# Optimization experiments

Measured on AMD Instinct MI355X. Metric: run time of the kernel, lower is better.

The kernel has to match this reference:

```python
import jax, jax.numpy as jnp
import numpy as np

STRIDE = 1
KSIZE = 3
DEMOD = True


def _conv_single(xi, wi, pad):
    # xi: [C,H,W], wi: [O,C,k,k] -> [O,H,W]
    out = jax.lax.conv_general_dilated(
        xi[None], wi, window_strides=(STRIDE, STRIDE),
        padding=[(pad, pad), (pad, pad)],
        dimension_numbers=("NCHW", "OIHW", "NCHW"))
    return out[0]


def setup_inputs() -> dict:
    key = jax.random.key(0)
    ks = jax.random.split(key, 6)
    B, Cin, Cout, S, H, W = 8, 512, 512, 512, 64, 64
    return {
        "x": jax.random.normal(ks[0], (B, Cin, H, W), jnp.float32),
        "y": jax.random.normal(ks[1], (B, S), jnp.float32),
        "affine_w": jax.random.normal(ks[2], (Cin, S), jnp.float32) * 0.02,
        "affine_b": jax.random.normal(ks[3], (Cin,), jnp.float32) * 0.02,
        "weight": jax.random.normal(ks[4], (Cout, Cin, KSIZE, KSIZE), jnp.float32) * 0.05,
        "bias": jax.random.normal(ks[5], (1, Cout, 1, 1), jnp.float32) * 0.02,
    }


def reference(x, y, affine_w, affine_b, weight, bias):
    B, _, H, W = x.shape
    style_dim = affine_w.shape[1]
    coef = 1.0 / np.sqrt(style_dim)  # ELR: gain / sqrt(fan_in)
    # style modulation scale per input channel: [B, Cin]
    s = (y * coef) @ affine_w.T + affine_b + 1.0
    # per-sample weights: [B, O, I, k, k]
    w = weight[None, :, :, :, :] * s[:, None, :, None, None]
    if DEMOD:
        d = jax.lax.rsqrt(jnp.sum(w * w, axis=(2, 3, 4), keepdims=True) + 1e-4)
        w = w * d
    pad = ((H - 1) * (STRIDE - 1) + (KSIZE - 1)) // 2
    out = jax.vmap(lambda xi, wi: _conv_single(xi, wi, pad))(x, w)  # [B,O,H,W]
    return out + bias
```

## Files before the change

kernel.cpp:

```cpp
#include <hip/hip_runtime.h>

typedef __attribute__((ext_vector_type(8))) short short8;
typedef __attribute__((ext_vector_type(4))) float floatx4;
typedef unsigned short u16;
typedef unsigned int u32;

#define NB 8
#define CI 512
#define CO 512
#define HH 64
#define WW 64
#define HP 66
#define WP 66
#define BK 64

__device__ __forceinline__ u16 f2bf(float f) {
  u32 u = __builtin_bit_cast(u32, f);
  u += 0x7fffu + ((u >> 16) & 1u);
  return (u16)(u >> 16);
}

__device__ __forceinline__ void gload16(const void* g, void* l) {
  __builtin_amdgcn_global_load_lds(
      (const __attribute__((address_space(1))) unsigned int*)g,
      (__attribute__((address_space(3))) unsigned int*)l, 16, 0, 0);
}

__global__ __launch_bounds__(256) void k_prep1(
    const float* __restrict__ y, const float* __restrict__ aw,
    const float* __restrict__ ab, float* __restrict__ s,
    const float* __restrict__ wt, float* __restrict__ wsum,
    u16* __restrict__ wbv)
{
  if (blockIdx.x < 1024) {
    const int wid = blockIdx.x * 4 + (threadIdx.x >> 6);
    const int lane = threadIdx.x & 63;
    const int b = wid >> 9, i = wid & 511;
    float sum = 0.f;
    #pragma unroll
    for (int j = 0; j < 8; ++j) {
      const int k = lane + (j << 6);
      sum += y[b * CI + k] * aw[i * CI + k];
    }
    #pragma unroll
    for (int off = 32; off; off >>= 1) sum += __shfl_xor(sum, off);
    if (lane == 0) s[wid] = sum * 0.044194173824159216f + ab[i] + 1.0f;
  } else {
    const int idx = (blockIdx.x - 1024) * 256 + threadIdx.x;
    const int i = idx & 511;
    const int o = idx >> 9;
    const float* p = wt + (size_t)idx * 9;
    float v[9];
    float sum = 0.f;
    #pragma unroll
    for (int t = 0; t < 9; ++t) { v[t] = p[t]; sum += v[t] * v[t]; }
    wsum[idx] = sum;
    #pragma unroll
    for (int t = 0; t < 9; ++t) wbv[(((o * 9 + t) << 9) | i)] = f2bf(v[t]);
  }
}

__global__ __launch_bounds__(256) void k_xfd(
    const float* __restrict__ x, const float* __restrict__ s,
    u16* __restrict__ xs, const float* __restrict__ wsum,
    float* __restrict__ d)
{
  __shared__ __align__(16) u16 lds[64 * 72];
  if (blockIdx.x >= 4096) {
    const int wid = (blockIdx.x - 4096) * 4 + (threadIdx.x >> 6);
    const int lane = threadIdx.x & 63;
    const int b = wid >> 9, o = wid & 511;
    float sum = 0.f;
    #pragma unroll
    for (int j = 0; j < 8; ++j) {
      const int i = lane + (j << 6);
      const float sv = s[b * CI + i];
      sum += wsum[o * CI + i] * sv * sv;
    }
    #pragma unroll
    for (int off = 32; off; off >>= 1) sum += __shfl_xor(sum, off);
    if (lane == 0) d[wid] = rsqrtf(sum + 1e-4f);
    return;
  }
  const int blk = blockIdx.x;
  const int ic = blk & 7;
  const int h = (blk >> 3) & 63;
  const int b = blk >> 9;
  const int i0 = ic << 6;
  const int t = threadIdx.x;
  const int w = t & 63;
  const int i4 = t >> 6;
  #pragma unroll
  for (int p = 0; p < 16; ++p) {
    const int ii = i4 + (p << 2);
    const float xv = x[((size_t)(b * CI + i0 + ii) * HH + h) * WW + w];
    const float sv = s[b * CI + i0 + ii];
    lds[w * 72 + ii] = f2bf(xv * sv);
  }
  const uint4 z4 = {0u, 0u, 0u, 0u};
  if (t < 16) {
    const int wside = (t < 8) ? 0 : 65;
    const int q = t & 7;
    *(uint4*)&xs[((size_t)(b * HP + h + 1) * WP + wside) * CI + i0 + (q << 3)] = z4;
  }
  if (h == 0) {
    for (int idx = t; idx < 2 * 66 * 8; idx += 256) {
      const int row = (idx < 528) ? 0 : 65;
      const int rem = (idx < 528) ? idx : idx - 528;
      const int wz = rem >> 3;
      const int q = rem & 7;
      *(uint4*)&xs[((size_t)(b * HP + row) * WP + wz) * CI + i0 + (q << 3)] = z4;
    }
  }
  __syncthreads();
  const int w2 = t >> 2;
  const int q = t & 3;
  const uint4* src = (const uint4*)&lds[w2 * 72 + (q << 4)];
  const uint4 v0 = src[0];
  const uint4 v1 = src[1];
  u16* dst = xs + ((size_t)(b * HP + h + 1) * WP + (w2 + 1)) * CI + i0 + (q << 4);
  *(uint4*)dst = v0;
  *((uint4*)dst + 1) = v1;
}

__global__ __launch_bounds__(512, 2) void k_conv(
    const u16* __restrict__ xs, const u16* __restrict__ wb,
    const float* __restrict__ dmod, const float* __restrict__ bias,
    float* __restrict__ out)
{
  __shared__ __align__(16) u16 lA[2 * 16384];
  __shared__ __align__(16) u16 lB[2 * 16384];

  const int blk0 = blockIdx.x;
  const int lblk = ((blk0 & 7) << 5) + (blk0 >> 3);
  const int mt = lblk >> 7;
  const int b  = (lblk >> 4) & 7;
  const int nt = lblk & 15;
  const int ob = mt << 8;
  const int p0 = nt << 8;

  const int tid = threadIdx.x;
  const int wid = tid >> 6;
  const int lane = tid & 63;
  const int col = lane & 15;
  const int k8  = lane >> 4;
  const int wr  = wid >> 2;
  const int wc  = wid & 3;

  const int lr = lane >> 3;
  const int ls = lane & 7;
  const int swz = ls ^ lr;

  u32 aoff[4], boff[4], ldst[4];
  #pragma unroll
  for (int h2 = 0; h2 < 4; ++h2) {
    const int rowBase = ((h2 >> 1) << 7) + (wid << 4) + ((h2 & 1) << 3);
    const int rowIdx = rowBase + lr;
    aoff[h2] = (u32)((ob + rowIdx) * 4608 + (swz << 3));
    const int p = p0 + rowIdx;
    boff[h2] = (u32)(((b * HP + (p >> 6)) * WP + (p & 63)) * 512 + (swz << 3));
    ldst[h2] = (u32)(rowBase << 6);
  }

  const u32 sA0 = (u32)(((0 + k8) ^ (col & 7)) << 3);
  const u32 sA1 = (u32)(((4 + k8) ^ (col & 7)) << 3);
  const u32 aRead = (u32)((((wr << 7) + col) << 6));
  const u32 bRead = (u32)((((wc << 6) + col) << 6));

  floatx4 acc[8][4];
  #pragma unroll
  for (int m = 0; m < 8; ++m)
    #pragma unroll
    for (int n = 0; n < 4; ++n)
      acc[m][n] = (floatx4){0.f, 0.f, 0.f, 0.f};

  short8 a0[4][2], b0[2][2], b1[2][2];

#define SA(TILE, H, BUF) do {                                                 \
    const u32 at_ = (u32)((TILE) << 6);                                       \
    gload16(wb + aoff[(H)*2+0] + at_, &lA[((BUF) << 14) + ldst[(H)*2+0]]);    \
    gload16(wb + aoff[(H)*2+1] + at_, &lA[((BUF) << 14) + ldst[(H)*2+1]]);    \
  } while (0)

#define SB(TILE, H, BUF) do {                                                 \
    const int t_ = (TILE);                                                    \
    const int tap_ = t_ >> 3;                                                 \
    const int kh_ = tap_ / 3;                                                 \
    const int kw_ = tap_ - kh_ * 3;                                           \
    const u32 bt_ = (u32)(((kh_ * WP + kw_) << 9) + ((t_ & 7) << 6));         \
    gload16(xs + boff[(H)*2+0] + bt_, &lB[((BUF) << 14) + ldst[(H)*2+0]]);    \
    gload16(xs + boff[(H)*2+1] + bt_, &lB[((BUF) << 14) + ldst[(H)*2+1]]);    \
  } while (0)

#define READ_A(PA, MH) do {                                                   \
    _Pragma("unroll")                                                         \
    for (int mq = 0; mq < 4; ++mq) {                                          \
      a0[mq][0] = *(const short8*)((PA) + (MH) * 4096 + mq * 1024 + sA0);     \
      a0[mq][1] = *(const short8*)((PA) + (MH) * 4096 + mq * 1024 + sA1);     \
    }                                                                         \
  } while (0)

#define READ_B(PB, NH, BV) do {                                               \
    _Pragma("unroll")                                                         \
    for (int nq = 0; nq < 2; ++nq) {                                          \
      BV[nq][0] = *(const short8*)((PB) + (NH) * 2048 + nq * 1024 + sA0);     \
      BV[nq][1] = *(const short8*)((PB) + (NH) * 2048 + nq * 1024 + sA1);     \
    }                                                                         \
  } while (0)

#define MFMA_Q(MH, NH, BV) do {                                               \
    _Pragma("unroll")                                                         \
    for (int kk = 0; kk < 2; ++kk)                                            \
      _Pragma("unroll")                                                       \
      for (int nq = 0; nq < 2; ++nq)                                          \
        _Pragma("unroll")                                                     \
        for (int mq = 0; mq < 4; ++mq)                                        \
          acc[(MH)*4+mq][(NH)*2+nq] = __builtin_amdgcn_mfma_f32_16x16x32_bf16(\
              a0[mq][kk], BV[nq][kk], acc[(MH)*4+mq][(NH)*2+nq], 0, 0, 0);    \
  } while (0)

#define SBAR __builtin_amdgcn_s_barrier()
#define SCH0 __builtin_amdgcn_sched_barrier(0)
#define PRI1 __builtin_amdgcn_s_setprio(1)
#define PRI0 __builtin_amdgcn_s_setprio(0)

#define BODY8(T0, FULL) do {                                                  \
    const u16* pA0 = lA + aRead;                                              \
    const u16* pB0 = lB + bRead;                                              \
    const u16* pA1 = lA + 16384 + aRead;                                      \
    const u16* pB1 = lB + 16384 + bRead;                                      \
                                        \
    READ_A(pA0, 0); READ_B(pB0, 0, b0);                                       \
    SCH0; SA((T0) + 1, 0, 1);                                                 \
    SBAR; PRI1; MFMA_Q(0, 0, b0); PRI0; SBAR;                                 \
                                                          \
    READ_B(pB0, 1, b1);                                                       \
    SCH0; SA((T0) + 1, 1, 1);                                                 \
    SBAR; PRI1; MFMA_Q(0, 1, b1); PRI0; SBAR;                                 \
                           \
    READ_A(pA0, 1);                                                           \
    SCH0; if (FULL) SB((T0) + 2, 0, 0);                                       \
    SBAR; PRI1; MFMA_Q(1, 1, b1); PRI0; SBAR;                                 \
                          \
    SCH0; if (FULL) SB((T0) + 2, 1, 0);                                       \
    SBAR; PRI1; MFMA_Q(1, 0, b0); PRI0;                                       \
    if (FULL) asm volatile("s_waitcnt vmcnt(4)" ::: "memory");                \
    else      asm volatile("s_waitcnt vmcnt(0)" ::: "memory");                \
    SBAR;                                                                     \
       \
    READ_A(pA1, 0); READ_B(pB1, 0, b0);                                       \
    SCH0; if (FULL) SA((T0) + 2, 0, 0);                                       \
    SBAR; PRI1; MFMA_Q(0, 0, b0); PRI0; SBAR;                                 \
                                                          \
    READ_B(pB1, 1, b1);                                                       \
    SCH0; if (FULL) SA((T0) + 2, 1, 0);                                       \
    SBAR; PRI1; MFMA_Q(0, 1, b1); PRI0; SBAR;                                 \
                           \
    READ_A(pA1, 1);                                                           \
    SCH0; if (FULL) SB((T0) + 3, 0, 1);                                       \
    SBAR; PRI1; MFMA_Q(1, 1, b1); PRI0; SBAR;                                 \
                          \
    SCH0; if (FULL) SB((T0) + 3, 1, 1);                                       \
    SBAR; PRI1; MFMA_Q(1, 0, b0); PRI0;                                       \
    if (FULL) asm volatile("s_waitcnt vmcnt(4)" ::: "memory");                \
    SBAR;                                                                     \
  } while (0)

  SB(0, 0, 0); SB(0, 1, 0); SA(0, 0, 0); SA(0, 1, 0);
  SB(1, 0, 1); SB(1, 1, 1);
  asm volatile("s_waitcnt vmcnt(4)" ::: "memory");
  SCH0;
  SBAR;

  for (int j = 0; j < 35; ++j) BODY8(j * 2, 1);
  BODY8(70, 0);

#undef SA
#undef SB
#undef READ_A
#undef READ_B
#undef MFMA_Q
#undef BODY8
#undef SBAR
#undef SCH0
#undef PRI1
#undef PRI0

  #pragma unroll
  for (int m = 0; m < 8; ++m) {
    #pragma unroll
    for (int r = 0; r < 4; ++r) {
      const int o = ob + (wr << 7) + (m << 4) + (k8 << 2) + r;
      const float dm = dmod[b * CO + o];
      const float bs = bias[o];
      float* po = out + (((size_t)(b * CO + o)) << 12) + p0 + (wc << 6);
      #pragma unroll
      for (int n = 0; n < 4; ++n)
        po[(n << 4) + col] = acc[m][n][r] * dm + bs;
    }
  }
}

extern "C" void kernel_launch(void* const* d_in, const int* in_sizes, int n_in,
                              void* d_out, int out_size, void* d_ws, size_t ws_size,
                              hipStream_t stream) {
  const float* x    = (const float*)d_in[0];
  const float* y    = (const float*)d_in[1];
  const float* aw   = (const float*)d_in[2];
  const float* ab   = (const float*)d_in[3];
  const float* wt   = (const float*)d_in[4];
  const float* bias = (const float*)d_in[5];
  float* out = (float*)d_out;

  char* ws = (char*)d_ws;
  const size_t XS_BYTES = (size_t)NB * HP * WP * CI * 2;
  const size_t WB_BYTES = (size_t)CO * 9 * CI * 2;
  const size_t WS_BYTES = (size_t)CO * CI * 4;
  u16* xsb    = (u16*)ws;
  u16* wbuf   = (u16*)(ws + XS_BYTES);
  float* wsum = (float*)(ws + XS_BYTES + WB_BYTES);
  float* sbuf = (float*)(ws + XS_BYTES + WB_BYTES + WS_BYTES);
  float* dbuf = sbuf + NB * CI;

  k_prep1<<<dim3(2048), dim3(256), 0, stream>>>(y, aw, ab, sbuf, wt, wsum, wbuf);
  k_xfd  <<<dim3(5120), dim3(256), 0, stream>>>(x, sbuf, xsb, wsum, dbuf);
  k_conv <<<dim3(256), dim3(512), 0, stream>>>(xsb, wbuf, dbuf, bias, out);
}
```

Measured before the change: 158.9 us.

## Restructure conv main loop into per-tile stages with early B prefetch

Rewrites the unrolled two-tile body into a TILE4 macro parameterised by buffer and mode. The next tile's first B fragment is read from LDS at the end of the current tile, and the vmcnt waits are split into finer stages. The block-index swizzle is also replaced with a plain linear mapping of (nt, mt, b). The aim is to hide LDS read latency before the first MFMA group. In exchange, the finer waits and the different B-buffer ordering risk race or stall issues, and dropping the swizzle may change L2 locality.

```diff
diff --git a/kernel.cpp b/kernel.cpp
--- a/kernel.cpp
+++ b/kernel.cpp
@@ -131,11 +131,10 @@
   __shared__ __align__(16) u16 lA[2 * 16384];
   __shared__ __align__(16) u16 lB[2 * 16384];
 
-  const int blk0 = blockIdx.x;
-  const int lblk = ((blk0 & 7) << 5) + (blk0 >> 3);
-  const int mt = lblk >> 7;
-  const int b  = (lblk >> 4) & 7;
-  const int nt = lblk & 15;
+  const int blk = blockIdx.x;
+  const int nt = blk & 15;
+  const int mt = (blk >> 4) & 1;
+  const int b  = blk >> 5;
   const int ob = mt << 8;
   const int p0 = nt << 8;
 
@@ -224,63 +223,57 @@
 #define PRI1 __builtin_amdgcn_s_setprio(1)
 #define PRI0 __builtin_amdgcn_s_setprio(0)
 
-#define BODY8(T0, FULL) do {                                                  \
-    const u16* pA0 = lA + aRead;                                              \
-    const u16* pB0 = lB + bRead;                                              \
-    const u16* pA1 = lA + 16384 + aRead;                                      \
-    const u16* pB1 = lB + 16384 + bRead;                                      \
-                                        \
-    READ_A(pA0, 0); READ_B(pB0, 0, b0);                                       \
-    SCH0; SA((T0) + 1, 0, 1);                                                 \
+#define TILE4(T, C, MODE) do {                                                \
+    const u16* pA  = lA + ((C) << 14) + aRead;                                \
+    const u16* pB  = lB + ((C) << 14) + bRead;                                \
+    const u16* pBn = lB + ((1 - (C)) << 14) + bRead;                          \
+         \
+    READ_A(pA, 0);                                                            \
+    SCH0; if (MODE >= 1) SA((T) + 1, 0, 1 - (C));                             \
     SBAR; PRI1; MFMA_Q(0, 0, b0); PRI0; SBAR;                                 \
-                                                          \
-    READ_B(pB0, 1, b1);                                                       \
-    SCH0; SA((T0) + 1, 1, 1);                                                 \
+                                     \
+    READ_B(pB, 1, b1);                                                        \
+    SCH0; if (MODE >= 1) SA((T) + 1, 1, 1 - (C));                             \
     SBAR; PRI1; MFMA_Q(0, 1, b1); PRI0; SBAR;                                 \
-                           \
-    READ_A(pA0, 1);                                                           \
-    SCH0; if (FULL) SB((T0) + 2, 0, 0);                                       \
+             \
+    READ_A(pA, 1);                                                            \
+    SCH0; if (MODE == 2) SB((T) + 2, 0, C);                                   \
+    if (MODE == 2)      asm volatile("s_waitcnt vmcnt(6)" ::: "memory");      \
+    else if (MODE == 1) asm volatile("s_waitcnt vmcnt(4)" ::: "memory");      \
     SBAR; PRI1; MFMA_Q(1, 1, b1); PRI0; SBAR;                                 \
-                          \
-    SCH0; if (FULL) SB((T0) + 2, 1, 0);                                       \
+                  \
+    SCH0; if (MODE == 2) SB((T) + 2, 1, C);                                   \
+    if (MODE == 2)      asm volatile("s_waitcnt vmcnt(4)" ::: "memory");      \
+    else if (MODE == 1) asm volatile("s_waitcnt vmcnt(0)" ::: "memory");      \
     SBAR; PRI1; MFMA_Q(1, 0, b0); PRI0;                                       \
-    if (FULL) asm volatile("s_waitcnt vmcnt(4)" ::: "memory");                \
-    else      asm volatile("s_waitcnt vmcnt(0)" ::: "memory");                \
+    if (MODE >= 1) READ_B(pBn, 0, b0);                                        \
     SBAR;                                                                     \
-       \
-    READ_A(pA1, 0); READ_B(pB1, 0, b0);                                       \
-    SCH0; if (FULL) SA((T0) + 2, 0, 0);                                       \
-    SBAR; PRI1; MFMA_Q(0, 0, b0); PRI0; SBAR;                                 \
-                                                          \
-    READ_B(pB1, 1, b1);                                                       \
-    SCH0; if (FULL) SA((T0) + 2, 1, 0);                                       \
-    SBAR; PRI1; MFMA_Q(0, 1, b1); PRI0; SBAR;                                 \
-                           \
-    READ_A(pA1, 1);                                                           \
-    SCH0; if (FULL) SB((T0) + 3, 0, 1);                                       \
-    SBAR; PRI1; MFMA_Q(1, 1, b1); PRI0; SBAR;                                 \
-                          \
-    SCH0; if (FULL) SB((T0) + 3, 1, 1);                                       \
-    SBAR; PRI1; MFMA_Q(1, 0, b0); PRI0;                                       \
-    if (FULL) asm volatile("s_waitcnt vmcnt(4)" ::: "memory");                \
-    SBAR;                                                                     \
-  } while (0)
-
-  SB(0, 0, 0); SB(0, 1, 0); SA(0, 0, 0); SA(0, 1, 0);
+  } while (0)
+
+  SB(0, 0, 0); SB(0, 1, 0);
+  SA(0, 0, 0); SA(0, 1, 0);
   SB(1, 0, 1); SB(1, 1, 1);
   asm volatile("s_waitcnt vmcnt(4)" ::: "memory");
   SCH0;
   SBAR;
-
-  for (int j = 0; j < 35; ++j) BODY8(j * 2, 1);
-  BODY8(70, 0);
+  {
+    const u16* pB0 = lB + bRead;
+    READ_B(pB0, 0, b0);
+  }
+
+  for (int j = 0; j < 35; ++j) {
+    TILE4(2 * j,     0, 2);
+    TILE4(2 * j + 1, 1, 2);
+  }
+  TILE4(70, 0, 1);
+  TILE4(71, 1, 0);
 
 #undef SA
 #undef SB
 #undef READ_A
 #undef READ_B
 #undef MFMA_Q
-#undef BODY8
+#undef TILE4
 #undef SBAR
 #undef SCH0
 #undef PRI1
```

New measurement: 154.2 us. 2.9% less time.
